# Performance work log

Hardware: AMD Instinct MI355X
Metric: run time of the kernel (lower is better)

## Reference

```python
import jax, jax.numpy as jnp
import numpy as np


def _pairwise_dist(x):
    # Euclidean (p=2) pairwise distances via Gram identity; avoids the
    # [N, N, D] broadcasted difference tensor the torch code materializes.
    sq = jnp.sum(x * x, axis=1)                      # [N]
    d2 = sq[:, None] + sq[None, :] - 2.0 * (x @ x.T)  # [N, N]
    return jnp.sqrt(jnp.clip(d2, 0.0))


def _persistence_pairs(dist_np):
    """0-dim persistent homology pairs = MST edges via Kruskal union-find,
    processed in order of increasing edge weight (matches the repo's
    PersistentHomologyCalculation). Returns [N-1, 2] int64 index pairs."""
    n = dist_np.shape[0]
    iu, ju = np.triu_indices(n, k=1)
    order = np.argsort(dist_np[iu, ju], kind='stable')
    parent = np.arange(n)

    def find(i):
        root = i
        while parent[root] != root:
            root = parent[root]
        while parent[i] != root:  # path compression
            parent[i], i = root, parent[i]
        return root

    pairs = []
    for e in order:
        a, b = find(iu[e]), find(ju[e])
        if a != b:
            parent[a] = b
            pairs.append((iu[e], ju[e]))
            if len(pairs) == n - 1:
                break
    return np.asarray(pairs, dtype=np.int64)


def setup_inputs() -> dict:
    key = jax.random.key(0)
    x = jax.random.normal(key, (2048, 4096), dtype=jnp.float32)
    return {"x": x}


def reference(x):
    distances = _pairwise_dist(x)  # [N, N]
    # Pair selection is done on host on detached values, as in the original
    # (pairs have fixed count N-1, so the output shape is static).
    pairs = _persistence_pairs(np.asarray(jax.device_get(distances)))
    i = jnp.asarray(pairs[:, 0])
    j = jnp.asarray(pairs[:, 1])
    selected_distances = distances[i, j]  # [N-1]
    return selected_distances
```

## Files before the change

### kernel.cpp

```cpp
#include <hip/hip_runtime.h>
#include <stdint.h>

#define NPTS 2048
#define KDIM 4096
#define INVALID_KEY 0xFFFFFFFFFFFFFFFFull

typedef __bf16 bf16x8 __attribute__((ext_vector_type(8)));
typedef float f32x4 __attribute__((ext_vector_type(4)));

__device__ __forceinline__ unsigned short f2bf(float f) {
    unsigned int u = __float_as_uint(f);
    u = (u + 0x7FFFu + ((u >> 16) & 1u)) >> 16;
    return (unsigned short)u;
}

__device__ __forceinline__ void gld_lds16(const unsigned short* g, unsigned short* l) {
    __builtin_amdgcn_global_load_lds(
        (const __attribute__((address_space(1))) unsigned int*)g,
        (__attribute__((address_space(3))) unsigned int*)l, 16, 0, 0);
}

__device__ __forceinline__ unsigned long long mk_key(float w, int i, int j) {
    unsigned long long a = (i < j) ? i : j;
    unsigned long long b = (i < j) ? j : i;
    return ((unsigned long long)__float_as_uint(w) << 22) | (a << 11) | b;
}

__global__ __launch_bounds__(256) void convert_sqnorm_kernel(const float* __restrict__ x,
                                                             unsigned short* __restrict__ xb,
                                                             float* __restrict__ sq,
                                                             int* __restrict__ comp0,
                                                             unsigned long long* __restrict__ best0,
                                                             int* __restrict__ ctl) {
    const int row = blockIdx.x;
    const float* xr = x + (size_t)row * KDIM;
    unsigned short* xbr = xb + (size_t)row * KDIM;
    const int t = threadIdx.x;
    float s = 0.f;
    #pragma unroll
    for (int k = 0; k < 4; ++k) {
        int c = t * 4 + k * 1024;
        float4 v = *(const float4*)(xr + c);
        s += v.x * v.x + v.y * v.y + v.z * v.z + v.w * v.w;
        uint2 u;
        u.x = (unsigned)f2bf(v.x) | ((unsigned)f2bf(v.y) << 16);
        u.y = (unsigned)f2bf(v.z) | ((unsigned)f2bf(v.w) << 16);
        *(uint2*)(xbr + c) = u;
    }
    for (int off = 32; off; off >>= 1) s += __shfl_down(s, off);
    __shared__ float p[4];
    if ((t & 63) == 0) p[t >> 6] = s;
    __syncthreads();
    if (t == 0) {
        sq[row] = p[0] + p[1] + p[2] + p[3];
        comp0[row] = row;
        best0[row] = INVALID_KEY;
        if (row == 0) { ctl[0] = 0; ctl[1] = 0; }
    }
}

__global__ __launch_bounds__(256, 2) void gemm_d2_glds(const unsigned short* __restrict__ xb,
                                                       const float* __restrict__ sq,
                                                       float* __restrict__ D2,
                                                       unsigned long long* __restrict__ best0) {
    __shared__ __align__(16) unsigned short tile[12 * 512];
    const int I0 = blockIdx.y * 64;
    const int J0 = blockIdx.x * 128;
    const int t = threadIdx.x;
    const int lane = t & 63;
    const int w = t >> 6;
    const int m = lane & 15, q = lane >> 4;

    const int rp = lane >> 2;
    const int sg = (lane & 3) ^ ((lane >> 3) & 3);
    const unsigned short* gsrc[3]; unsigned short* ldst[3];
    #pragma unroll
    for (int ci = 0; ci < 3; ++ci) {
        int c = w * 3 + ci;
        int rowbase = (c < 4) ? (I0 + c * 16) : (J0 + (c - 4) * 16);
        gsrc[ci] = xb + (size_t)(rowbase + rp) * KDIM + sg * 8;
        ldst[ci] = tile + c * 512;
    }
    const int fro = m * 32 + ((q ^ ((m >> 1) & 3)) * 8);

    f32x4 acc[4][2] = {};
    for (int kc = 0; kc < KDIM; kc += 32) {
        #pragma unroll
        for (int ci = 0; ci < 3; ++ci) gld_lds16(gsrc[ci] + kc, ldst[ci]);
        __syncthreads();
        bf16x8 af[4], bg[2];
        #pragma unroll
        for (int rt = 0; rt < 4; ++rt)
            af[rt] = *(const bf16x8*)(tile + rt * 512 + fro);
        #pragma unroll
        for (int ct = 0; ct < 2; ++ct)
            bg[ct] = *(const bf16x8*)(tile + (4 + w * 2 + ct) * 512 + fro);
        #pragma unroll
        for (int rt = 0; rt < 4; ++rt)
            #pragma unroll
            for (int ct = 0; ct < 2; ++ct)
                acc[rt][ct] = __builtin_amdgcn_mfma_f32_16x16x32_bf16(
                    af[rt], bg[ct], acc[rt][ct], 0, 0, 0);
        __syncthreads();
    }

    unsigned long long* s_best = (unsigned long long*)tile;
    if (t < 64) s_best[t] = INVALID_KEY;
    __syncthreads();
    #pragma unroll
    for (int rt = 0; rt < 4; ++rt) {
        #pragma unroll
        for (int r = 0; r < 4; ++r) {
            int i = I0 + rt * 16 + q * 4 + r;
            unsigned long long kk = INVALID_KEY;
            #pragma unroll
            for (int ct = 0; ct < 2; ++ct) {
                int j = J0 + w * 32 + ct * 16 + m;
                float v = sq[i] + sq[j] - 2.0f * acc[rt][ct][r];
                v = (i == j) ? __builtin_inff() : fmaxf(v, 0.0f);
                D2[(size_t)i * NPTS + j] = v;
                if (i != j) {
                    unsigned long long key = mk_key(v, i, j);
                    kk = (key < kk) ? key : kk;
                }
            }
            #pragma unroll
            for (int mask = 1; mask < 16; mask <<= 1) {
                unsigned long long o = __shfl_xor(kk, mask);
                kk = (o < kk) ? o : kk;
            }
            if (m == 0) atomicMin(&s_best[rt * 16 + q * 4 + r], kk);
        }
    }
    __syncthreads();
    if (t < 64) atomicMin(&best0[I0 + t], s_best[t]);
}

__global__ __launch_bounds__(256) void boruvka_round(const float* __restrict__ D2,
                                                     const unsigned long long* __restrict__ bestP,
                                                     unsigned long long* __restrict__ bestN,
                                                     const int* __restrict__ compP,
                                                     int* __restrict__ compN,
                                                     float* __restrict__ ew,
                                                     int* __restrict__ ctl) {
    if (ctl[1]) return;
    __shared__ int sc[NPTS];
    __shared__ unsigned long long compBest[NPTS];
    __shared__ int par[NPTS];
    __shared__ int s_wsum[4];
    __shared__ int s_nroots;
    const int t = threadIdx.x;
    const int bid = blockIdx.x;
    const int lane = t & 63, w = t >> 6;

    if (t == 0) s_nroots = 0;
    #pragma unroll
    for (int e = 0; e < 8; ++e) {
        int v = t * 8 + e;
        sc[v] = compP[v];
        compBest[v] = INVALID_KEY;
    }
    __syncthreads();

    unsigned long long kreg[8]; int oreg[8];
    #pragma unroll
    for (int e = 0; e < 8; ++e) {
        int v = t * 8 + e;
        unsigned long long k = bestP[v];
        kreg[e] = k;
        int a = (int)((k >> 11) & 2047), b = (int)(k & 2047);
        oreg[e] = (a == v) ? b : a;
        if (k != INVALID_KEY && sc[oreg[e]] != sc[v])
            atomicMin(&compBest[sc[v]], k);
    }
    __syncthreads();

    bool isr[8];
    #pragma unroll
    for (int e = 0; e < 8; ++e) {
        int c = t * 8 + e;
        int p = c;
        isr[e] = (sc[c] == c);
        if (isr[e]) {
            unsigned long long k = compBest[c];
            if (k != INVALID_KEY) {
                int a = (int)((k >> 11) & 2047), b = (int)(k & 2047);
                int j = (sc[a] == c) ? b : a;
                int rj = sc[j];
                bool mutual = (compBest[rj] == k);
                if (!(mutual && c < rj)) {
                    p = rj;
                    if (bid == 0)
                        ew[atomicAdd(&ctl[0], 1)] = __uint_as_float((unsigned)(k >> 22));
                }
            }
        }
        par[c] = p;
    }
    int any = __syncthreads_or(1);
    do {
        int local = 0;
        #pragma unroll
        for (int e = 0; e < 8; ++e) {
            if (isr[e]) {
                int c = t * 8 + e;
                int p = par[c];
                int np = par[p];
                if (np != p) { par[c] = np; local = 1; }
            }
        }
        any = __syncthreads_or(local);
    } while (any);

    int newsc[8]; int rc = 0;
    #pragma unroll
    for (int e = 0; e < 8; ++e) {
        int v = t * 8 + e;
        newsc[e] = par[sc[v]];
        if (newsc[e] == v) rc++;
    }
    if (rc) atomicAdd(&s_nroots, rc);
    __syncthreads();
    #pragma unroll
    for (int e = 0; e < 8; ++e) sc[t * 8 + e] = newsc[e];
    __syncthreads();
    const int nroots = s_nroots;

    if (bid == 0) {
        #pragma unroll
        for (int e = 0; e < 8; ++e) compN[t * 8 + e] = newsc[e];
        if (t == 0 && nroots == 1) ctl[1] = 1;
    }
    if (nroots == 1) return;

    int flags[8], lc = 0;
    #pragma unroll
    for (int e = 0; e < 8; ++e) {
        int v = t * 8 + e;
        flags[e] = (kreg[e] == INVALID_KEY) || (sc[oreg[e]] == sc[v]);
        lc += flags[e];
    }
    int scn = lc;
    #pragma unroll
    for (int d = 1; d < 64; d <<= 1) {
        int o = __shfl_up(scn, d);
        if (lane >= d) scn += o;
    }
    if (lane == 63) s_wsum[w] = scn;
    __syncthreads();
    int wbase = 0;
    for (int i = 0; i < w; ++i) wbase += s_wsum[i];
    const int cnt = s_wsum[0] + s_wsum[1] + s_wsum[2] + s_wsum[3];
    int base = wbase + scn - lc;
    int* rlist = par;
    #pragma unroll
    for (int e = 0; e < 8; ++e)
        if (flags[e]) rlist[base++] = t * 8 + e;
    __syncthreads();

    if (t < 4) {
        int v = bid * 4 + t;
        unsigned long long k = bestP[v];
        if (k != INVALID_KEY) {
            int a = (int)((k >> 11) & 2047), b = (int)(k & 2047);
            int o = (a == v) ? b : a;
            if (sc[o] != sc[v]) bestN[v] = k;
        }
    }
    int widx = bid * 4 + w;
    if (widx < cnt) {
        int v = rlist[widx];
        int mc = sc[v];
        const float* row = D2 + (size_t)v * NPTS;
        unsigned long long best = INVALID_KEY;
        #pragma unroll
        for (int k = 0; k < 8; ++k) {
            int j0 = k * 256 + lane * 4;
            float4 w4 = *(const float4*)(row + j0);
            int4 c4 = *(const int4*)(sc + j0);
            float wa[4] = {w4.x, w4.y, w4.z, w4.w};
            int ca[4] = {c4.x, c4.y, c4.z, c4.w};
            #pragma unroll
            for (int e = 0; e < 4; ++e) {
                if (ca[e] != mc) {
                    unsigned long long key = mk_key(wa[e], v, j0 + e);
                    best = (key < best) ? key : best;
                }
            }
        }
        for (int off = 32; off; off >>= 1) {
            unsigned long long o = __shfl_down(best, off);
            best = (o < best) ? o : best;
        }
        if (lane == 0) bestN[v] = best;
    }
}

__global__ __launch_bounds__(1024) void sort_out_kernel(const float* __restrict__ ew,
                                                        float* __restrict__ out) {
    __shared__ float wl[NPTS];
    const int t = threadIdx.x;
    for (int i = t; i < NPTS; i += 1024)
        wl[i] = (i < NPTS - 1) ? ew[i] : __builtin_inff();
    __syncthreads();
    for (int k = 2; k <= NPTS; k <<= 1) {
        for (int j = k >> 1; j > 0; j >>= 1) {
            for (int i = t; i < NPTS; i += 1024) {
                int l = i ^ j;
                if (l > i) {
                    float a = wl[i], b = wl[l];
                    bool up = ((i & k) == 0);
                    if ((a > b) == up) { wl[i] = b; wl[l] = a; }
                }
            }
            __syncthreads();
        }
    }
    for (int i = t; i < NPTS - 1; i += 1024)
        out[i] = sqrtf(fmaxf(wl[i], 0.0f));
}

extern "C" void kernel_launch(void* const* d_in, const int* in_sizes, int n_in,
                              void* d_out, int out_size, void* d_ws, size_t ws_size,
                              hipStream_t stream) {
    const float* x = (const float*)d_in[0];
    float* out = (float*)d_out;
    char* ws = (char*)d_ws;
    unsigned short* xb = (unsigned short*)ws;
    float* D2 = (float*)(ws + 16777216);
    size_t o = 33554432;
    float* sq = (float*)(ws + o);                  o += 8192;
    unsigned long long* best0 = (unsigned long long*)(ws + o); o += 16384;
    unsigned long long* best1 = (unsigned long long*)(ws + o); o += 16384;
    int* comp0 = (int*)(ws + o);                   o += 8192;
    int* comp1 = (int*)(ws + o);                   o += 8192;
    float* ew = (float*)(ws + o);                  o += 8192;
    int* ctl = (int*)(ws + o);

    hipLaunchKernelGGL(convert_sqnorm_kernel, dim3(NPTS), dim3(256), 0, stream,
                       x, xb, sq, comp0, best0, ctl);
    hipLaunchKernelGGL(gemm_d2_glds, dim3(16, 32), dim3(256), 0, stream,
                       xb, sq, D2, best0);
    for (int r = 0; r < 11; ++r) {
        unsigned long long* bp = (r & 1) ? best1 : best0;
        unsigned long long* bn = (r & 1) ? best0 : best1;
        int* cp = (r & 1) ? comp1 : comp0;
        int* cn = (r & 1) ? comp0 : comp1;
        hipLaunchKernelGGL(boruvka_round, dim3(512), dim3(256), 0, stream,
                           D2, bp, bn, cp, cn, ew, ctl);
    }
    hipLaunchKernelGGL(sort_out_kernel, dim3(1), dim3(1024), 0, stream, ew, out);
}
```

Before: 232.0 us.

## Double-buffer LDS tiles with K=64 stages in the distance GEMM

The bf16 Gram GEMM now double-buffers its LDS tiles. Each stage loads two 32-wide K slices, and the async global-to-LDS load for the next stage is issued before the MFMA work on the current buffer. This aims to hide global load latency and halve the number of barriers per K step, at the cost of four times the LDS per block, which could limit occupancy. A prologue and epilogue handle the first and last stages.

```diff
diff --git a/kernel.cpp b/kernel.cpp
--- a/kernel.cpp
+++ b/kernel.cpp
@@ -63,7 +63,7 @@
                                                        const float* __restrict__ sq,
                                                        float* __restrict__ D2,
                                                        unsigned long long* __restrict__ best0) {
-    __shared__ __align__(16) unsigned short tile[12 * 512];
+    __shared__ __align__(16) unsigned short tile[2 * 12288];
     const int I0 = blockIdx.y * 64;
     const int J0 = blockIdx.x * 128;
     const int t = threadIdx.x;
@@ -73,36 +73,63 @@
 
     const int rp = lane >> 2;
     const int sg = (lane & 3) ^ ((lane >> 3) & 3);
-    const unsigned short* gsrc[3]; unsigned short* ldst[3];
-    #pragma unroll
-    for (int ci = 0; ci < 3; ++ci) {
-        int c = w * 3 + ci;
-        int rowbase = (c < 4) ? (I0 + c * 16) : (J0 + (c - 4) * 16);
-        gsrc[ci] = xb + (size_t)(rowbase + rp) * KDIM + sg * 8;
-        ldst[ci] = tile + c * 512;
-    }
+    const unsigned short* gsrc[6]; int ldoff[6];
+    #pragma unroll
+    for (int s = 0; s < 2; ++s)
+        #pragma unroll
+        for (int ci = 0; ci < 3; ++ci) {
+            int c = w * 3 + ci;
+            int rowbase = (c < 4) ? (I0 + c * 16) : (J0 + (c - 4) * 16);
+            int idx = s * 3 + ci;
+            gsrc[idx] = xb + (size_t)(rowbase + rp) * KDIM + s * 32 + sg * 8;
+            ldoff[idx] = (s * 12 + c) * 512;
+        }
     const int fro = m * 32 + ((q ^ ((m >> 1) & 3)) * 8);
 
     f32x4 acc[4][2] = {};
-    for (int kc = 0; kc < KDIM; kc += 32) {
-        #pragma unroll
-        for (int ci = 0; ci < 3; ++ci) gld_lds16(gsrc[ci] + kc, ldst[ci]);
+    unsigned short* buf0 = tile;
+    unsigned short* buf1 = tile + 12288;
+
+    auto STAGE = [&](unsigned short* base, int kc) {
+        #pragma unroll
+        for (int idx = 0; idx < 6; ++idx)
+            gld_lds16(gsrc[idx] + kc, base + ldoff[idx]);
+    };
+    auto COMPUTE = [&](const unsigned short* base) {
+        #pragma unroll
+        for (int s = 0; s < 2; ++s) {
+            bf16x8 af[4], bg[2];
+            #pragma unroll
+            for (int rt = 0; rt < 4; ++rt)
+                af[rt] = *(const bf16x8*)(base + (s * 12 + rt) * 512 + fro);
+            #pragma unroll
+            for (int ct = 0; ct < 2; ++ct)
+                bg[ct] = *(const bf16x8*)(base + (s * 12 + 4 + w * 2 + ct) * 512 + fro);
+            #pragma unroll
+            for (int rt = 0; rt < 4; ++rt)
+                #pragma unroll
+                for (int ct = 0; ct < 2; ++ct)
+                    acc[rt][ct] = __builtin_amdgcn_mfma_f32_16x16x32_bf16(
+                        af[rt], bg[ct], acc[rt][ct], 0, 0, 0);
+        }
+    };
+
+    STAGE(buf0, 0);
+    __syncthreads();
+    #pragma unroll 1
+    for (int kc = 64; kc < KDIM - 64; kc += 128) {
+        STAGE(buf1, kc);
+        COMPUTE(buf0);
         __syncthreads();
-        bf16x8 af[4], bg[2];
-        #pragma unroll
-        for (int rt = 0; rt < 4; ++rt)
-            af[rt] = *(const bf16x8*)(tile + rt * 512 + fro);
-        #pragma unroll
-        for (int ct = 0; ct < 2; ++ct)
-            bg[ct] = *(const bf16x8*)(tile + (4 + w * 2 + ct) * 512 + fro);
-        #pragma unroll
-        for (int rt = 0; rt < 4; ++rt)
-            #pragma unroll
-            for (int ct = 0; ct < 2; ++ct)
-                acc[rt][ct] = __builtin_amdgcn_mfma_f32_16x16x32_bf16(
-                    af[rt], bg[ct], acc[rt][ct], 0, 0, 0);
+        STAGE(buf0, kc + 64);
+        COMPUTE(buf1);
         __syncthreads();
     }
+    STAGE(buf1, KDIM - 64);
+    COMPUTE(buf0);
+    __syncthreads();
+    COMPUTE(buf1);
+    __syncthreads();
 
     unsigned long long* s_best = (unsigned long long*)tile;
     if (t < 64) s_best[t] = INVALID_KEY;
```

New measurement: 218.2 us. 6.0% less time.
